# Performance work log

Hardware: AMD Instinct MI355X
Metric: run time of the kernel (lower is better)

Reference implementation:

```python
import jax, jax.numpy as jnp
import numpy as np

NUM_HEADS = 8
GROUPS = 32
EPS = 1e-5


def group_norm(x, gamma, beta):
    # x: (b, c, L)
    b, c, L = x.shape
    xg = x.reshape(b, GROUPS, c // GROUPS, L)
    mean = xg.mean(axis=(2, 3), keepdims=True)
    var = xg.var(axis=(2, 3), keepdims=True)
    xn = ((xg - mean) / jnp.sqrt(var + EPS)).reshape(b, c, L)
    return xn * gamma[None, :, None] + beta[None, :, None]


def setup_inputs() -> dict:
    key = jax.random.key(0)
    ks = jax.random.split(key, 8)
    b, c, h, w = 8, 512, 32, 32
    inner = c  # inner_channels == -1 -> channels
    x = jax.random.normal(ks[0], (b, c, h, w), dtype=jnp.float32)
    gamma = jnp.ones((c,), dtype=jnp.float32)
    beta = jnp.zeros((c,), dtype=jnp.float32)
    Wq = jax.random.normal(ks[1], (inner, c), dtype=jnp.float32) * 0.02
    bq = jnp.zeros((inner,), dtype=jnp.float32)
    Wkv = jax.random.normal(ks[2], (2 * inner, c), dtype=jnp.float32) * 0.02
    bkv = jnp.zeros((2 * inner,), dtype=jnp.float32)
    Wo = jax.random.normal(ks[3], (c, inner), dtype=jnp.float32) * 0.02
    bo = jnp.zeros((c,), dtype=jnp.float32)
    return {"x": x, "gamma": gamma, "beta": beta, "Wq": Wq, "bq": bq,
            "Wkv": Wkv, "bkv": bkv, "Wo": Wo, "bo": bo}


def reference(x, gamma, beta, Wq, bq, Wkv, bkv, Wo, bo):
    b, c = x.shape[:2]
    spatial = x.shape[2:]
    L = int(np.prod(spatial))
    inner = Wq.shape[0]
    dh = inner // NUM_HEADS
    scale = dh ** -0.5  # NOTE: applied to BOTH q and k, as in the source

    xr = x.reshape(b, c, L)
    hn = group_norm(xr, gamma, beta)          # norm(x); also serves as context

    # 1x1 Conv1d == channel matmul
    q = jnp.einsum('oc,bcl->bol', Wq, hn) + bq[None, :, None]
    kv = jnp.einsum('oc,bcl->bol', Wkv, hn) + bkv[None, :, None]
    k, v = jnp.split(kv, 2, axis=1)

    # (b, heads, dh, L)
    qh = (q * scale).reshape(b, NUM_HEADS, dh, L)
    kh = (k * scale).reshape(b, NUM_HEADS, dh, L)
    vh = v.reshape(b, NUM_HEADS, dh, L)

    dots = jnp.einsum('bhdt,bhds->bhts', qh, kh)
    attn = jax.nn.softmax(dots.astype(jnp.float32), axis=-1).astype(dots.dtype)
    out = jnp.einsum('bhts,bhds->bhdt', attn, vh)  # (b, heads, dh, L)

    out = out.reshape(b, inner, L)
    # output Linear over the channel dim
    out = jnp.einsum('oc,bcl->bol', Wo, out) + bo[None, :, None]
    return (xr + out).reshape(b, c, *spatial)
```

## Files before the change

kernel.cpp:

```cpp
#include <hip/hip_runtime.h>
#include <math.h>

#define B_ 8
#define C_ 512
#define L_ 1024
#define NH_ 8
#define DH_ 64
#define EPS 1e-5f
#define SCALE 0.125f
#define QSCALE (0.125f * 1.44269504088896f)

typedef __bf16 bf16x8 __attribute__((ext_vector_type(8)));
typedef __bf16 bf16x4 __attribute__((ext_vector_type(4)));
typedef float  f32x4  __attribute__((ext_vector_type(4)));
typedef float  f32x16 __attribute__((ext_vector_type(16)));

#define MFMA16(a, b, c) __builtin_amdgcn_mfma_f32_16x16x32_bf16((a), (b), (c), 0, 0, 0)
#define MFMA32(a, b, c) __builtin_amdgcn_mfma_f32_32x32x16_bf16((a), (b), (c), 0, 0, 0)

__device__ __forceinline__ void glds16(const __bf16* g, __bf16* l) {
    __builtin_amdgcn_global_load_lds((const __attribute__((address_space(1))) void*)(g),
                                     (__attribute__((address_space(3))) void*)(l),
                                     16, 0, 0);
}

__global__ __launch_bounds__(256)
void prep_kernel(const float* __restrict__ Wq, const float* __restrict__ Wkv,
                 const float* __restrict__ Wo, __bf16* __restrict__ dst,
                 const float* __restrict__ x, float* __restrict__ stats) {
    __shared__ float rs[256], rss[256];
    int bid = blockIdx.x, tid = threadIdx.x;
    if (bid < 1024) {
        int idx = bid * 256 + tid;
        float4 v;
        if (idx < 65536)        v = ((const float4*)Wq)[idx];
        else if (idx < 196608)  v = ((const float4*)Wkv)[idx - 65536];
        else                    v = ((const float4*)Wo)[idx - 196608];
        bf16x4 o;
        o[0] = (__bf16)v.x; o[1] = (__bf16)v.y; o[2] = (__bf16)v.z; o[3] = (__bf16)v.w;
        ((bf16x4*)dst)[idx] = o;
        return;
    }
    int bg = bid - 1024;
    size_t goff = (size_t)bg * 16 * L_;
    const float4* x4 = (const float4*)(x + goff);
    float s = 0.f, ss = 0.f;
    for (int i = tid; i < 4096; i += 256) {
        float4 v = x4[i];
        s  += v.x + v.y + v.z + v.w;
        ss += v.x * v.x + v.y * v.y + v.z * v.z + v.w * v.w;
    }
    rs[tid] = s; rss[tid] = ss;
    __syncthreads();
    for (int off = 128; off > 0; off >>= 1) {
        if (tid < off) { rs[tid] += rs[tid + off]; rss[tid] += rss[tid + off]; }
        __syncthreads();
    }
    if (tid == 0) {
        const float inv_n = 1.f / 16384.f;
        float mean = rs[0] * inv_n;
        float var  = rss[0] * inv_n - mean * mean;
        stats[bg * 2]     = mean;
        stats[bg * 2 + 1] = rsqrtf(var + EPS);
    }
}

__global__ __launch_bounds__(256)
void gn_apply_kernel(const float* __restrict__ x, const float* __restrict__ gamma,
                     const float* __restrict__ beta, const float* __restrict__ stats,
                     __bf16* __restrict__ hnT) {
    __shared__ __bf16 T[32 * 520];
    const int lt = blockIdx.x, b = blockIdx.y;
    const int tid = threadIdx.x;
    const int l0 = lt * 32;
    const int cbase = tid >> 3, fl = tid & 7;
#pragma unroll
    for (int p = 0; p < 16; ++p) {
        int cc = cbase + p * 32;
        float4 v = *(const float4*)&x[((size_t)b * C_ + cc) * L_ + l0 + fl * 4];
        int bg = b * 32 + (cc >> 4);
        float m = stats[bg * 2], rstd = stats[bg * 2 + 1];
        float ga = gamma[cc] * rstd, be = beta[cc];
        T[(fl * 4 + 0) * 520 + cc] = (__bf16)((v.x - m) * ga + be);
        T[(fl * 4 + 1) * 520 + cc] = (__bf16)((v.y - m) * ga + be);
        T[(fl * 4 + 2) * 520 + cc] = (__bf16)((v.z - m) * ga + be);
        T[(fl * 4 + 3) * 520 + cc] = (__bf16)((v.w - m) * ga + be);
    }
    __syncthreads();
    const int lrow = tid >> 6, cu = tid & 63;
#pragma unroll
    for (int pp = 0; pp < 8; ++pp) {
        int l = pp * 4 + lrow;
        bf16x8 r = *(const bf16x8*)&T[l * 520 + cu * 8];
        *(bf16x8*)&hnT[((size_t)b * L_ + l0 + l) * C_ + cu * 8] = r;
    }
}

__device__ __forceinline__
void gemm_mainloop(const __bf16* __restrict__ A, const __bf16* __restrict__ Bp,
                   __bf16* As, __bf16* Bs, f32x4 acc[4][4]) {
    const int tid = threadIdx.x;
    const int lane = tid & 63, w = tid >> 6;
    const int c = lane & 15, q = lane >> 4;
    const int wm = (w >> 1) * 64, wn = (w & 1) * 64;
    const int l8 = lane >> 3, kgsw = (lane & 7) ^ l8;

#pragma unroll
    for (int buf = 0; buf < 2; ++buf)
#pragma unroll
        for (int i = 0; i < 4; ++i) {
            int chunk = w * 4 + i;
            int row = chunk * 8 + l8;
            glds16(A  + (size_t)row * 512 + buf * 64 + kgsw * 8, &As[buf * 8192 + chunk * 512]);
            glds16(Bp + (size_t)row * 512 + buf * 64 + kgsw * 8, &Bs[buf * 8192 + chunk * 512]);
        }
    asm volatile("s_waitcnt vmcnt(8)" ::: "memory");
    asm volatile("s_barrier" ::: "memory");

    for (int it = 0; it < 8; ++it) {
        const __bf16* Ac = As + (it & 1) * 8192;
        const __bf16* Bc = Bs + (it & 1) * 8192;
#pragma unroll
        for (int ks = 0; ks < 2; ++ks) {
            const int koff = ((ks * 4 + q) ^ (c & 7)) * 8;
            bf16x8 af[4], bfr[4];
#pragma unroll
            for (int m = 0; m < 4; ++m)
                af[m] = *(const bf16x8*)&Ac[(wm + m * 16 + c) * 64 + koff];
#pragma unroll
            for (int n = 0; n < 4; ++n)
                bfr[n] = *(const bf16x8*)&Bc[(wn + n * 16 + c) * 64 + koff];
#pragma unroll
            for (int m = 0; m < 4; ++m)
#pragma unroll
                for (int n = 0; n < 4; ++n)
                    acc[m][n] = MFMA16(af[m], bfr[n], acc[m][n]);
        }
        asm volatile("s_barrier" ::: "memory");
        if (it < 6) {
            int k0n = (it + 2) * 64;
#pragma unroll
            for (int i = 0; i < 4; ++i) {
                int chunk = w * 4 + i;
                int row = chunk * 8 + l8;
                glds16(A  + (size_t)row * 512 + k0n + kgsw * 8, &As[(it & 1) * 8192 + chunk * 512]);
                glds16(Bp + (size_t)row * 512 + k0n + kgsw * 8, &Bs[(it & 1) * 8192 + chunk * 512]);
            }
            asm volatile("s_waitcnt vmcnt(8)" ::: "memory");
        } else {
            asm volatile("s_waitcnt vmcnt(0)" ::: "memory");
        }
        asm volatile("s_barrier" ::: "memory");
    }
}

__global__ __launch_bounds__(256)
void qkv_kernel(const __bf16* __restrict__ Wq_bf, const __bf16* __restrict__ Wkv_bf,
                const __bf16* __restrict__ hnT,
                const float* __restrict__ bq, const float* __restrict__ bkv,
                __bf16* __restrict__ qT, __bf16* __restrict__ kT,
                __bf16* __restrict__ vv) {
    __shared__ __bf16 SMEM[128 * 64 * 4];
    __bf16* As = SMEM;
    __bf16* Bs = SMEM + 16384;
    const int bid = blockIdx.x;
    const int wgid = (bid & 7) * 96 + (bid >> 3);
    const int b = wgid / 96;
    const int xx = wgid % 96;
    const int sec = xx >> 5, t = xx & 31;
    const __bf16* hb = hnT + (size_t)b * L_ * C_;

    const __bf16 *A, *Bp;
    int m0, n0;
    if (sec < 2) {
        m0 = (t & 3) * 128; n0 = (t >> 2) * 128;
        A  = (sec == 0 ? Wq_bf : Wkv_bf) + (size_t)m0 * 512;
        Bp = hb + (size_t)n0 * 512;
    } else {
        m0 = (t >> 2) * 128; n0 = (t & 3) * 128;
        A  = hb + (size_t)m0 * 512;
        Bp = Wkv_bf + (size_t)(512 + n0) * 512;
    }

    f32x4 acc[4][4];
#pragma unroll
    for (int m = 0; m < 4; ++m)
#pragma unroll
        for (int n = 0; n < 4; ++n)
#pragma unroll
            for (int r = 0; r < 4; ++r) acc[m][n][r] = 0.f;

    gemm_mainloop(A, Bp, As, Bs, acc);

    const int tid = threadIdx.x, lane = tid & 63, w = tid >> 6;
    const int c = lane & 15, q = lane >> 4;
    const int wm = (w >> 1) * 64, wn = (w & 1) * 64;

    __bf16* T2 = SMEM;
    const float* bias = (sec == 0) ? bq : bkv;
    const float scl = (sec == 0) ? QSCALE : SCALE;
#pragma unroll
    for (int mt = 0; mt < 4; ++mt)
#pragma unroll
        for (int nt = 0; nt < 4; ++nt) {
            int n_loc = wn + nt * 16 + c;
            int u4 = (wm >> 2) + mt * 4 + q;
            int u4sw = u4 ^ ((n_loc & 7) << 1);
            bf16x4 ov;
            if (sec < 2) {
                int ob = m0 + wm + mt * 16 + q * 4;
#pragma unroll
                for (int r = 0; r < 4; ++r)
                    ov[r] = (__bf16)((acc[mt][nt][r] + bias[ob + r]) * scl);
            } else {
                float bi = bkv[512 + n0 + n_loc];
#pragma unroll
                for (int r = 0; r < 4; ++r)
                    ov[r] = (__bf16)(acc[mt][nt][r] + bi);
            }
            *(bf16x4*)&T2[n_loc * 128 + u4sw * 4] = ov;
        }
    __syncthreads();
#pragma unroll
    for (int p = 0; p < 8; ++p) {
        int rrow = p * 16 + (tid >> 4);
        int u16 = tid & 15;
        int u4p = (u16 * 2) ^ ((rrow & 7) << 1);
        bf16x8 val = *(const bf16x8*)&T2[rrow * 128 + u4p * 4];
        if (sec < 2) {
            int l = n0 + rrow;
            int og = m0 + u16 * 8;
            int hh = og >> 6, d0 = og & 63;
            __bf16* dstp = (sec == 0) ? qT : kT;
            *(bf16x8*)&dstp[((size_t)(b * NH_ + hh) * L_ + l) * DH_ + d0] = val;
        } else {
            int o = n0 + rrow;
            int lg = m0 + u16 * 8;
            *(bf16x8*)&vv[((size_t)b * C_ + o) * L_ + lg] = val;
        }
    }
}

__global__ __launch_bounds__(256, 2)
void attn_kernel(const __bf16* __restrict__ qT, const __bf16* __restrict__ kT,
                 const __bf16* __restrict__ vv, __bf16* __restrict__ aoT) {
    const int bid = blockIdx.x;
    const int wg = (bid & 7) * 64 + (bid >> 3);
    const int tt = wg & 7, h = (wg >> 3) & 7, b = wg >> 6;
    const int t0 = tt * 128;
    __shared__ __bf16 Qs[128 * 64];
    __shared__ __bf16 Ks[2][64 * 64];
    __shared__ __bf16 Vs[2][64 * 64];

    const int tid = threadIdx.x, lane = tid & 63, w = tid >> 6;
    const int l8 = lane >> 3, kg = (lane & 7) ^ l8;
    const int ln = lane & 31, hi = lane >> 5, r7 = ln & 7;

    const __bf16* qbase = qT + ((size_t)(b * NH_ + h) * L_ + t0) * DH_;
    const __bf16* kbase = kT + (size_t)(b * NH_ + h) * L_ * DH_;
    const __bf16* vbase = vv + (size_t)(b * C_ + h * DH_) * L_;

#pragma unroll
    for (int i = 0; i < 4; ++i) {
        int chunk = w * 4 + i;
        glds16(qbase + (size_t)(chunk * 8 + l8) * DH_ + kg * 8, &Qs[chunk * 512]);
    }
#pragma unroll
    for (int buf = 0; buf < 2; ++buf)
#pragma unroll
        for (int i = 0; i < 2; ++i) {
            int chunk = w * 2 + i, row = chunk * 8 + l8;
            glds16(kbase + (size_t)(buf * 64 + row) * DH_ + kg * 8, &Ks[buf][chunk * 512]);
            glds16(vbase + (size_t)row * L_ + buf * 64 + kg * 8, &Vs[buf][chunk * 512]);
        }
    asm volatile("s_waitcnt vmcnt(4)" ::: "memory");
    asm volatile("s_barrier" ::: "memory");

    f32x16 o_acc[2];
#pragma unroll
    for (int dt = 0; dt < 2; ++dt)
#pragma unroll
        for (int r = 0; r < 16; ++r) o_acc[dt][r] = 0.f;
    float l_own = 0.f;

    const int qrow = w * 32 + ln;

    for (int it = 0; it < 16; ++it) {
        const __bf16* Kc = Ks[it & 1];
        const __bf16* Vc = Vs[it & 1];

        f32x16 sres[2];
#pragma unroll
        for (int mt = 0; mt < 2; ++mt)
#pragma unroll
            for (int r = 0; r < 16; ++r) sres[mt][r] = 0.f;
        __builtin_amdgcn_s_setprio(1);
#pragma unroll
        for (int ks = 0; ks < 4; ++ks) {
            bf16x8 bQ = *(const bf16x8*)&Qs[qrow * 64 + ((ks * 2 + hi) ^ r7) * 8];
#pragma unroll
            for (int mt = 0; mt < 2; ++mt) {
                bf16x8 aK = *(const bf16x8*)&Kc[(mt * 32 + ln) * 64 + ((ks * 2 + hi) ^ r7) * 8];
                sres[mt] = MFMA32(aK, bQ, sres[mt]);
            }
        }
        __builtin_amdgcn_s_setprio(0);

        bf16x8 frag[4];
#pragma unroll
        for (int mt = 0; mt < 2; ++mt) {
            float pv[16];
#pragma unroll
            for (int r = 0; r < 16; ++r) pv[r] = exp2f(sres[mt][r]);
            float s0a = (pv[0] + pv[1]) + (pv[2] + pv[3]);
            float s1a = (pv[4] + pv[5]) + (pv[6] + pv[7]);
            float s2a = (pv[8] + pv[9]) + (pv[10] + pv[11]);
            float s3a = (pv[12] + pv[13]) + (pv[14] + pv[15]);
            l_own += (s0a + s1a) + (s2a + s3a);
            unsigned int P[8];
#pragma unroll
            for (int j = 0; j < 8; ++j)
                asm("v_cvt_pk_bf16_f32 %0, %1, %2" : "=v"(P[j]) : "v"(pv[2 * j]), "v"(pv[2 * j + 1]));
            asm("v_permlane32_swap_b32 %0, %1" : "+v"(P[0]), "+v"(P[2]));
            asm("v_permlane32_swap_b32 %0, %1" : "+v"(P[1]), "+v"(P[3]));
            asm("v_permlane32_swap_b32 %0, %1" : "+v"(P[4]), "+v"(P[6]));
            asm("v_permlane32_swap_b32 %0, %1" : "+v"(P[5]), "+v"(P[7]));
            union FU { unsigned int u[4]; bf16x8 v; } fa, fb;
            fa.u[0] = P[0]; fa.u[1] = P[1]; fa.u[2] = P[2]; fa.u[3] = P[3];
            fb.u[0] = P[4]; fb.u[1] = P[5]; fb.u[2] = P[6]; fb.u[3] = P[7];
            frag[mt * 2 + 0] = fa.v;
            frag[mt * 2 + 1] = fb.v;
        }

        __builtin_amdgcn_s_setprio(1);
#pragma unroll
        for (int ks2 = 0; ks2 < 4; ++ks2) {
#pragma unroll
            for (int dt = 0; dt < 2; ++dt) {
                bf16x8 aV = *(const bf16x8*)&Vc[(dt * 32 + ln) * 64 + ((ks2 * 2 + hi) ^ r7) * 8];
                o_acc[dt] = MFMA32(aV, frag[ks2], o_acc[dt]);
            }
        }
        __builtin_amdgcn_s_setprio(0);

        asm volatile("s_barrier" ::: "memory");
        if (it < 14) {
            int s0n = (it + 2) * 64;
#pragma unroll
            for (int i = 0; i < 2; ++i) {
                int chunk = w * 2 + i, row = chunk * 8 + l8;
                glds16(kbase + (size_t)(s0n + row) * DH_ + kg * 8, &Ks[it & 1][chunk * 512]);
                glds16(vbase + (size_t)row * L_ + s0n + kg * 8, &Vs[it & 1][chunk * 512]);
            }
            asm volatile("s_waitcnt vmcnt(4)" ::: "memory");
        } else {
            asm volatile("s_waitcnt vmcnt(0)" ::: "memory");
        }
        asm volatile("s_barrier" ::: "memory");
    }

    float l_tot = l_own + __shfl_xor(l_own, 32);
    float linv = 1.f / l_tot;
    const int tg = t0 + w * 32 + ln;
    __bf16* aobase = aoT + ((size_t)b * L_ + tg) * C_ + h * DH_;
#pragma unroll
    for (int dt = 0; dt < 2; ++dt)
#pragma unroll
        for (int rq = 0; rq < 4; ++rq) {
            bf16x4 ov;
#pragma unroll
            for (int j = 0; j < 4; ++j) ov[j] = (__bf16)(o_acc[dt][rq * 4 + j] * linv);
            *(bf16x4*)&aobase[dt * 32 + rq * 8 + hi * 4] = ov;
        }
}

__global__ __launch_bounds__(256)
void proj_kernel(const __bf16* __restrict__ aoT, const __bf16* __restrict__ Wo_bf,
                 const float* __restrict__ bo, const float* __restrict__ x,
                 float* __restrict__ out) {
    __shared__ __bf16 As[2 * 8192], Bs[2 * 8192];
    const int bid = blockIdx.x;
    const int wgid = (bid & 7) * 32 + (bid >> 3);
    const int b = wgid >> 5, t = wgid & 31;
    const int m0 = (t >> 2) * 128;
    const int n0 = (t & 3) * 128;
    const __bf16* A  = aoT + (size_t)b * L_ * C_ + (size_t)m0 * 512;
    const __bf16* Bp = Wo_bf + (size_t)n0 * 512;

    f32x4 acc[4][4];
#pragma unroll
    for (int m = 0; m < 4; ++m)
#pragma unroll
        for (int n = 0; n < 4; ++n)
#pragma unroll
            for (int r = 0; r < 4; ++r) acc[m][n][r] = 0.f;

    gemm_mainloop(A, Bp, As, Bs, acc);

    const int tid = threadIdx.x, lane = tid & 63, w = tid >> 6;
    const int c = lane & 15, q = lane >> 4;
    const int wm = (w >> 1) * 64, wn = (w & 1) * 64;

#pragma unroll
    for (int mt = 0; mt < 4; ++mt)
#pragma unroll
        for (int nt = 0; nt < 4; ++nt) {
            int lb = m0 + wm + mt * 16 + q * 4;
            int o  = n0 + wn + nt * 16 + c;
            float bi = bo[o];
            size_t off = ((size_t)b * C_ + o) * L_ + lb;
            float4 xv = *(const float4*)&x[off];
            float4 rv;
            rv.x = acc[mt][nt][0] + bi + xv.x;
            rv.y = acc[mt][nt][1] + bi + xv.y;
            rv.z = acc[mt][nt][2] + bi + xv.z;
            rv.w = acc[mt][nt][3] + bi + xv.w;
            *(float4*)&out[off] = rv;
        }
}

extern "C" void kernel_launch(void* const* d_in, const int* in_sizes, int n_in,
                              void* d_out, int out_size, void* d_ws, size_t ws_size,
                              hipStream_t stream) {
    const float* x     = (const float*)d_in[0];
    const float* gamma = (const float*)d_in[1];
    const float* beta  = (const float*)d_in[2];
    const float* Wq    = (const float*)d_in[3];
    const float* bq    = (const float*)d_in[4];
    const float* Wkv   = (const float*)d_in[5];
    const float* bkv   = (const float*)d_in[6];
    const float* Wo    = (const float*)d_in[7];
    const float* bo    = (const float*)d_in[8];
    float* out = (float*)d_out;

    __bf16* wsb = (__bf16*)d_ws;
    __bf16* Wq_bf  = wsb;
    __bf16* Wkv_bf = wsb + 262144;
    __bf16* Wo_bf  = wsb + 786432;
    __bf16* hnT    = wsb + 1048576;
    __bf16* qT     = wsb + 5242880;
    __bf16* kT     = wsb + 9437184;
    __bf16* vv     = wsb + 13631488;
    __bf16* aoT    = wsb + 17825792;
    float*  stats  = (float*)(wsb + 22020096);

    prep_kernel<<<dim3(1280), 256, 0, stream>>>(Wq, Wkv, Wo, wsb, x, stats);
    gn_apply_kernel<<<dim3(32, B_), 256, 0, stream>>>(x, gamma, beta, stats, hnT);
    qkv_kernel<<<dim3(768), 256, 0, stream>>>(Wq_bf, Wkv_bf, hnT, bq, bkv, qT, kT, vv);
    attn_kernel<<<dim3(512), 256, 0, stream>>>(qT, kT, vv, aoT);
    proj_kernel<<<dim3(256), 256, 0, stream>>>(aoT, Wo_bf, bo, x, out);
}
```

Baseline: 160.8 us.

## Triple-buffer K/V tiles, keep Q in registers, compute row sums via MFMA

Measured after the change: 160.5 us. Within noise of the previous version (-0.2%).

```diff
diff --git a/kernel.cpp b/kernel.cpp
--- a/kernel.cpp
+++ b/kernel.cpp
@@ -249,8 +249,8 @@
     const int tt = wg & 7, h = (wg >> 3) & 7, b = wg >> 6;
     const int t0 = tt * 128;
     __shared__ __bf16 Qs[128 * 64];
-    __shared__ __bf16 Ks[2][64 * 64];
-    __shared__ __bf16 Vs[2][64 * 64];
+    __shared__ __bf16 Ks[3][64 * 64];
+    __shared__ __bf16 Vs[3][64 * 64];
 
     const int tid = threadIdx.x, lane = tid & 63, w = tid >> 6;
     const int l8 = lane >> 3, kg = (lane & 7) ^ l8;
@@ -276,18 +276,30 @@
     asm volatile("s_waitcnt vmcnt(4)" ::: "memory");
     asm volatile("s_barrier" ::: "memory");
 
-    f32x16 o_acc[2];
+    const int qrow = w * 32 + ln;
+    bf16x8 qf[4];
+#pragma unroll
+    for (int ks = 0; ks < 4; ++ks)
+        qf[ks] = *(const bf16x8*)&Qs[qrow * 64 + ((ks * 2 + hi) ^ r7) * 8];
+
+    bf16x8 aOnes;
+    {
+        __bf16 one = (__bf16)((ln == 0) ? 1.f : 0.f);
+#pragma unroll
+        for (int j = 0; j < 8; ++j) aOnes[j] = one;
+    }
+
+    f32x16 o_acc[2], o_l;
 #pragma unroll
     for (int dt = 0; dt < 2; ++dt)
 #pragma unroll
         for (int r = 0; r < 16; ++r) o_acc[dt][r] = 0.f;
-    float l_own = 0.f;
-
-    const int qrow = w * 32 + ln;
+#pragma unroll
+    for (int r = 0; r < 16; ++r) o_l[r] = 0.f;
 
     for (int it = 0; it < 16; ++it) {
-        const __bf16* Kc = Ks[it & 1];
-        const __bf16* Vc = Vs[it & 1];
+        const __bf16* Kc = &Ks[0][0] + (it % 3) * 4096;
+        const __bf16* Vc = &Vs[0][0] + (it % 3) * 4096;
 
         f32x16 sres[2];
 #pragma unroll
@@ -297,11 +309,10 @@
         __builtin_amdgcn_s_setprio(1);
 #pragma unroll
         for (int ks = 0; ks < 4; ++ks) {
-            bf16x8 bQ = *(const bf16x8*)&Qs[qrow * 64 + ((ks * 2 + hi) ^ r7) * 8];
 #pragma unroll
             for (int mt = 0; mt < 2; ++mt) {
                 bf16x8 aK = *(const bf16x8*)&Kc[(mt * 32 + ln) * 64 + ((ks * 2 + hi) ^ r7) * 8];
-                sres[mt] = MFMA32(aK, bQ, sres[mt]);
+                sres[mt] = MFMA32(aK, qf[ks], sres[mt]);
             }
         }
         __builtin_amdgcn_s_setprio(0);
@@ -312,11 +323,6 @@
             float pv[16];
 #pragma unroll
             for (int r = 0; r < 16; ++r) pv[r] = exp2f(sres[mt][r]);
-            float s0a = (pv[0] + pv[1]) + (pv[2] + pv[3]);
-            float s1a = (pv[4] + pv[5]) + (pv[6] + pv[7]);
-            float s2a = (pv[8] + pv[9]) + (pv[10] + pv[11]);
-            float s3a = (pv[12] + pv[13]) + (pv[14] + pv[15]);
-            l_own += (s0a + s1a) + (s2a + s3a);
             unsigned int P[8];
 #pragma unroll
             for (int j = 0; j < 8; ++j)
@@ -340,27 +346,30 @@
                 bf16x8 aV = *(const bf16x8*)&Vc[(dt * 32 + ln) * 64 + ((ks2 * 2 + hi) ^ r7) * 8];
                 o_acc[dt] = MFMA32(aV, frag[ks2], o_acc[dt]);
             }
+            o_l = MFMA32(aOnes, frag[ks2], o_l);
         }
         __builtin_amdgcn_s_setprio(0);
 
-        asm volatile("s_barrier" ::: "memory");
-        if (it < 14) {
+        if (it <= 13) {
             int s0n = (it + 2) * 64;
+            __bf16* Kw = &Ks[0][0] + ((it + 2) % 3) * 4096;
+            __bf16* Vw = &Vs[0][0] + ((it + 2) % 3) * 4096;
 #pragma unroll
             for (int i = 0; i < 2; ++i) {
                 int chunk = w * 2 + i, row = chunk * 8 + l8;
-                glds16(kbase + (size_t)(s0n + row) * DH_ + kg * 8, &Ks[it & 1][chunk * 512]);
-                glds16(vbase + (size_t)row * L_ + s0n + kg * 8, &Vs[it & 1][chunk * 512]);
+                glds16(kbase + (size_t)(s0n + row) * DH_ + kg * 8, &Kw[chunk * 512]);
+                glds16(vbase + (size_t)row * L_ + s0n + kg * 8, &Vw[chunk * 512]);
             }
             asm volatile("s_waitcnt vmcnt(4)" ::: "memory");
-        } else {
+            asm volatile("s_barrier" ::: "memory");
+        } else if (it == 14) {
             asm volatile("s_waitcnt vmcnt(0)" ::: "memory");
-        }
-        asm volatile("s_barrier" ::: "memory");
-    }
-
-    float l_tot = l_own + __shfl_xor(l_own, 32);
-    float linv = 1.f / l_tot;
+            asm volatile("s_barrier" ::: "memory");
+        }
+    }
+
+    float lsum = __shfl(o_l[0], ln);
+    float linv = 1.f / lsum;
     const int tg = t0 + w * 32 + ln;
     __bf16* aobase = aoT + ((size_t)b * L_ + tg) * C_ + h * DH_;
 #pragma unroll
```
